# Performance work log

Hardware: AMD Instinct MI355X
Metric: run time of the kernel (lower is better)

The kernel has to match this reference:

```python
import jax, jax.numpy as jnp
import numpy as np
from jax import lax

BN_EPS = 1e-5


def setup_inputs() -> dict:
    key = jax.random.key(0)
    k = jax.random.split(key, 7)
    B, H, W = 128, 224, 224
    return {
        "x": jax.random.normal(k[0], (B, 1, H, W), dtype=jnp.float32),
        "conv_w": jax.random.normal(k[1], (16, 1, 5, 5), dtype=jnp.float32) * 0.1,
        "conv_b": jax.random.normal(k[2], (16,), dtype=jnp.float32) * 0.1,
        "gamma": jax.random.uniform(k[3], (16,), dtype=jnp.float32, minval=0.5, maxval=1.5),
        "beta": jax.random.normal(k[4], (16,), dtype=jnp.float32) * 0.1,
        "run_mean": jax.random.normal(k[5], (16,), dtype=jnp.float32) * 0.1,
        "run_var": jax.random.uniform(k[6], (16,), dtype=jnp.float32, minval=0.5, maxval=1.5),
    }


def reference(x, conv_w, conv_b, gamma, beta, run_mean, run_var):
    # Conv2d(1,16,5,stride=1,padding=2): NCHW x OIHW -> NCHW
    y = lax.conv_general_dilated(
        x, conv_w, window_strides=(1, 1), padding=[(2, 2), (2, 2)],
        dimension_numbers=("NCHW", "OIHW", "NCHW"))
    y = y + conv_b[None, :, None, None]
    # BatchNorm2d(16) in inference form with running stats
    scale = gamma * lax.rsqrt(run_var + BN_EPS)
    y = y * scale[None, :, None, None] + (beta - run_mean * scale)[None, :, None, None]
    # ReLU
    y = jnp.maximum(y, 0.0)
    # MaxPool2d(kernel=2, stride=2)
    out = lax.reduce_window(y, -jnp.inf, lax.max,
                            window_dimensions=(1, 1, 2, 2),
                            window_strides=(1, 1, 2, 2),
                            padding="VALID")
    return out  # [B, 16, H/2, W/2]
```

## Files before the change

kernel.cpp:

```cpp
#include <hip/hip_runtime.h>
#include <stdint.h>

#define TILE_P 16
#define TILE_C 32
#define HALO 2
#define IN_TILE 36
#define IMG 224
#define OUT_DIM 112
#define NCH 16

typedef __fp16 half2_t __attribute__((ext_vector_type(2)));

#define WS_WPAIRS 32

__global__ void prep_kernel(const float* __restrict__ conv_w,
                            const float* __restrict__ conv_b,
                            const float* __restrict__ gamma,
                            const float* __restrict__ beta,
                            const float* __restrict__ run_mean,
                            const float* __restrict__ run_var,
                            uint32_t* __restrict__ ws)
{
    int ch = threadIdx.x;
    if (ch >= NCH) return;
    float s = gamma[ch] * rsqrtf(run_var[ch] + 1e-5f);
    float t = fmaf(s, conv_b[ch] - run_mean[ch], beta[ch]);
    float2* st = (float2*)ws;
    st[ch] = make_float2(s, t);

    uint32_t* wp = ws + WS_WPAIRS + ch * 20;
    const float* w = conv_w + ch * 25;
    for (int r = 0; r < 5; ++r) {
        half2_t A = __builtin_amdgcn_cvt_pkrtz(w[r*5+0], w[r*5+1]);
        half2_t B = __builtin_amdgcn_cvt_pkrtz(w[r*5+2], w[r*5+3]);
        half2_t C = __builtin_amdgcn_cvt_pkrtz(w[r*5+4], 0.f);
        half2_t D = __builtin_amdgcn_cvt_pkrtz(0.f, w[r*5+4]);
        wp[r*4+0] = __builtin_bit_cast(uint32_t, A);
        wp[r*4+1] = __builtin_bit_cast(uint32_t, B);
        wp[r*4+2] = __builtin_bit_cast(uint32_t, C);
        wp[r*4+3] = __builtin_bit_cast(uint32_t, D);
    }
}

__global__ __launch_bounds__(256, 4)
void conv_bn_relu_pool(const float* __restrict__ x,
                       const uint32_t* __restrict__ ws,
                       float* __restrict__ out)
{
    __shared__ float smem[IN_TILE * IN_TILE];
    const int tid = threadIdx.x;
    const int b  = blockIdx.z;
    const int ty = blockIdx.y * TILE_C;
    const int tx = blockIdx.x * TILE_C;

    const float* xb = x + (size_t)b * IMG * IMG;

    for (int i = tid; i < IN_TILE * IN_TILE; i += 256) {
        int r = i / IN_TILE, c = i - r * IN_TILE;
        int gy = ty - HALO + r, gx = tx - HALO + c;
        float v = 0.f;
        if ((unsigned)gy < IMG && (unsigned)gx < IMG) v = xb[gy * IMG + gx];
        smem[i] = v;
    }
    __syncthreads();

    const int px = tid & 15;
    const int py = tid >> 4;

    const int base = (py * 2) * IN_TILE + px * 2;
    half2_t h2[6][5];
    #pragma unroll
    for (int r = 0; r < 6; ++r) {
        float p0 = smem[base + r * IN_TILE + 0];
        float p1 = smem[base + r * IN_TILE + 1];
        float p2 = smem[base + r * IN_TILE + 2];
        float p3 = smem[base + r * IN_TILE + 3];
        float p4 = smem[base + r * IN_TILE + 4];
        float p5 = smem[base + r * IN_TILE + 5];
        h2[r][0] = __builtin_amdgcn_cvt_pkrtz(p0, p1);
        h2[r][1] = __builtin_amdgcn_cvt_pkrtz(p1, p2);
        h2[r][2] = __builtin_amdgcn_cvt_pkrtz(p2, p3);
        h2[r][3] = __builtin_amdgcn_cvt_pkrtz(p3, p4);
        h2[r][4] = __builtin_amdgcn_cvt_pkrtz(p4, p5);
    }

    const int oy = blockIdx.y * TILE_P + py;
    const int ox = blockIdx.x * TILE_P + px;
    float* outb = out + (size_t)b * NCH * (OUT_DIM * OUT_DIM) + oy * OUT_DIM + ox;

    const float2* st = (const float2*)ws;

    #pragma unroll
    for (int ch = 0; ch < NCH; ++ch) {
        const uint32_t* wp = ws + WS_WPAIRS + ch * 20;
        float a00 = 0.f, a01 = 0.f, a10 = 0.f, a11 = 0.f;
        #pragma unroll
        for (int r = 0; r < 5; ++r) {
            half2_t A = __builtin_bit_cast(half2_t, wp[r*4+0]);
            half2_t B = __builtin_bit_cast(half2_t, wp[r*4+1]);
            half2_t C = __builtin_bit_cast(half2_t, wp[r*4+2]);
            half2_t D = __builtin_bit_cast(half2_t, wp[r*4+3]);
            a00 = __builtin_amdgcn_fdot2(h2[r][0], A, a00, false);
            a00 = __builtin_amdgcn_fdot2(h2[r][2], B, a00, false);
            a00 = __builtin_amdgcn_fdot2(h2[r][4], C, a00, false);
            a01 = __builtin_amdgcn_fdot2(h2[r][1], A, a01, false);
            a01 = __builtin_amdgcn_fdot2(h2[r][3], B, a01, false);
            a01 = __builtin_amdgcn_fdot2(h2[r][4], D, a01, false);
            a10 = __builtin_amdgcn_fdot2(h2[r+1][0], A, a10, false);
            a10 = __builtin_amdgcn_fdot2(h2[r+1][2], B, a10, false);
            a10 = __builtin_amdgcn_fdot2(h2[r+1][4], C, a10, false);
            a11 = __builtin_amdgcn_fdot2(h2[r+1][1], A, a11, false);
            a11 = __builtin_amdgcn_fdot2(h2[r+1][3], B, a11, false);
            a11 = __builtin_amdgcn_fdot2(h2[r+1][4], D, a11, false);
        }
        float m = fmaxf(fmaxf(a00, a01), fmaxf(a10, a11));
        float2 s_t = st[ch];
        float y = fmaxf(fmaf(m, s_t.x, s_t.y), 0.f);
        outb[ch * (OUT_DIM * OUT_DIM)] = y;
    }
}

extern "C" void kernel_launch(void* const* d_in, const int* in_sizes, int n_in,
                              void* d_out, int out_size, void* d_ws, size_t ws_size,
                              hipStream_t stream) {
    const float* x        = (const float*)d_in[0];
    const float* conv_w   = (const float*)d_in[1];
    const float* conv_b   = (const float*)d_in[2];
    const float* gamma    = (const float*)d_in[3];
    const float* beta     = (const float*)d_in[4];
    const float* run_mean = (const float*)d_in[5];
    const float* run_var  = (const float*)d_in[6];
    float* out = (float*)d_out;
    uint32_t* ws = (uint32_t*)d_ws;

    prep_kernel<<<1, 64, 0, stream>>>(conv_w, conv_b, gamma, beta, run_mean, run_var, ws);

    dim3 grid(IMG / TILE_C, IMG / TILE_C, 128);
    dim3 block(256);
    conv_bn_relu_pool<<<grid, block, 0, stream>>>(x, ws, out);
}
```

Measured before the change: 175.0 us.

## Precompute packed fp16 pixel pairs in LDS and process channels in groups

The block now converts the input tile once into a shared table of packed fp16 adjacent-pixel pairs, instead of each thread converting its own overlapping 6x6 window. The channel loop is restructured into four non-unrolled groups of four channels; within each group the thread reloads its pairs from LDS per filter row. The launch-bounds occupancy hint is also dropped. The aim is to cut redundant conversions and register pressure, at the cost of an extra barrier, more LDS space and repeated LDS reads across groups.

```diff
diff --git a/kernel.cpp b/kernel.cpp
--- a/kernel.cpp
+++ b/kernel.cpp
@@ -8,6 +8,7 @@
 #define IMG 224
 #define OUT_DIM 112
 #define NCH 16
+#define PAIR_STRIDE 40
 
 typedef __fp16 half2_t __attribute__((ext_vector_type(2)));
 
@@ -42,12 +43,18 @@
     }
 }
 
-__global__ __launch_bounds__(256, 4)
+__device__ __forceinline__ half2_t ld_pair(const uint32_t* p) {
+    return __builtin_bit_cast(half2_t, *p);
+}
+
+__global__ __launch_bounds__(256)
 void conv_bn_relu_pool(const float* __restrict__ x,
                        const uint32_t* __restrict__ ws,
                        float* __restrict__ out)
 {
-    __shared__ float smem[IN_TILE * IN_TILE];
+    __shared__ float T[IN_TILE * IN_TILE];
+    __shared__ uint32_t P[IN_TILE * PAIR_STRIDE];
+
     const int tid = threadIdx.x;
     const int b  = blockIdx.z;
     const int ty = blockIdx.y * TILE_C;
@@ -60,29 +67,20 @@
         int gy = ty - HALO + r, gx = tx - HALO + c;
         float v = 0.f;
         if ((unsigned)gy < IMG && (unsigned)gx < IMG) v = xb[gy * IMG + gx];
-        smem[i] = v;
+        T[i] = v;
+    }
+    __syncthreads();
+
+    for (int i = tid; i < IN_TILE * (IN_TILE - 1); i += 256) {
+        int r = i / (IN_TILE - 1), c = i - r * (IN_TILE - 1);
+        half2_t h = __builtin_amdgcn_cvt_pkrtz(T[r * IN_TILE + c], T[r * IN_TILE + c + 1]);
+        P[r * PAIR_STRIDE + c] = __builtin_bit_cast(uint32_t, h);
     }
     __syncthreads();
 
     const int px = tid & 15;
     const int py = tid >> 4;
-
-    const int base = (py * 2) * IN_TILE + px * 2;
-    half2_t h2[6][5];
-    #pragma unroll
-    for (int r = 0; r < 6; ++r) {
-        float p0 = smem[base + r * IN_TILE + 0];
-        float p1 = smem[base + r * IN_TILE + 1];
-        float p2 = smem[base + r * IN_TILE + 2];
-        float p3 = smem[base + r * IN_TILE + 3];
-        float p4 = smem[base + r * IN_TILE + 4];
-        float p5 = smem[base + r * IN_TILE + 5];
-        h2[r][0] = __builtin_amdgcn_cvt_pkrtz(p0, p1);
-        h2[r][1] = __builtin_amdgcn_cvt_pkrtz(p1, p2);
-        h2[r][2] = __builtin_amdgcn_cvt_pkrtz(p2, p3);
-        h2[r][3] = __builtin_amdgcn_cvt_pkrtz(p3, p4);
-        h2[r][4] = __builtin_amdgcn_cvt_pkrtz(p4, p5);
-    }
+    const uint32_t* prow = P + (2 * py) * PAIR_STRIDE + 2 * px;
 
     const int oy = blockIdx.y * TILE_P + py;
     const int ox = blockIdx.x * TILE_P + px;
@@ -90,33 +88,54 @@
 
     const float2* st = (const float2*)ws;
 
-    #pragma unroll
-    for (int ch = 0; ch < NCH; ++ch) {
-        const uint32_t* wp = ws + WS_WPAIRS + ch * 20;
-        float a00 = 0.f, a01 = 0.f, a10 = 0.f, a11 = 0.f;
+    #pragma unroll 1
+    for (int g = 0; g < 4; ++g) {
+        const uint32_t* wp = ws + WS_WPAIRS + g * 80;
+        float acc[4][4];
+        #pragma unroll
+        for (int i = 0; i < 4; ++i)
+            #pragma unroll
+            for (int j = 0; j < 4; ++j) acc[i][j] = 0.f;
+
         #pragma unroll
         for (int r = 0; r < 5; ++r) {
-            half2_t A = __builtin_bit_cast(half2_t, wp[r*4+0]);
-            half2_t B = __builtin_bit_cast(half2_t, wp[r*4+1]);
-            half2_t C = __builtin_bit_cast(half2_t, wp[r*4+2]);
-            half2_t D = __builtin_bit_cast(half2_t, wp[r*4+3]);
-            a00 = __builtin_amdgcn_fdot2(h2[r][0], A, a00, false);
-            a00 = __builtin_amdgcn_fdot2(h2[r][2], B, a00, false);
-            a00 = __builtin_amdgcn_fdot2(h2[r][4], C, a00, false);
-            a01 = __builtin_amdgcn_fdot2(h2[r][1], A, a01, false);
-            a01 = __builtin_amdgcn_fdot2(h2[r][3], B, a01, false);
-            a01 = __builtin_amdgcn_fdot2(h2[r][4], D, a01, false);
-            a10 = __builtin_amdgcn_fdot2(h2[r+1][0], A, a10, false);
-            a10 = __builtin_amdgcn_fdot2(h2[r+1][2], B, a10, false);
-            a10 = __builtin_amdgcn_fdot2(h2[r+1][4], C, a10, false);
-            a11 = __builtin_amdgcn_fdot2(h2[r+1][1], A, a11, false);
-            a11 = __builtin_amdgcn_fdot2(h2[r+1][3], B, a11, false);
-            a11 = __builtin_amdgcn_fdot2(h2[r+1][4], D, a11, false);
+            const uint32_t* p0 = prow + r * PAIR_STRIDE;
+            const uint32_t* p1 = p0 + PAIR_STRIDE;
+            half2_t q00 = ld_pair(p0 + 0), q01 = ld_pair(p0 + 1);
+            half2_t q02 = ld_pair(p0 + 2), q03 = ld_pair(p0 + 3);
+            half2_t q04 = ld_pair(p0 + 4);
+            half2_t q10 = ld_pair(p1 + 0), q11 = ld_pair(p1 + 1);
+            half2_t q12 = ld_pair(p1 + 2), q13 = ld_pair(p1 + 3);
+            half2_t q14 = ld_pair(p1 + 4);
+            #pragma unroll
+            for (int i = 0; i < 4; ++i) {
+                half2_t A = __builtin_bit_cast(half2_t, wp[i*20 + r*4 + 0]);
+                half2_t B = __builtin_bit_cast(half2_t, wp[i*20 + r*4 + 1]);
+                half2_t C = __builtin_bit_cast(half2_t, wp[i*20 + r*4 + 2]);
+                half2_t D = __builtin_bit_cast(half2_t, wp[i*20 + r*4 + 3]);
+                acc[i][0] = __builtin_amdgcn_fdot2(q00, A,
+                            __builtin_amdgcn_fdot2(q02, B,
+                            __builtin_amdgcn_fdot2(q04, C, acc[i][0], false), false), false);
+                acc[i][1] = __builtin_amdgcn_fdot2(q01, A,
+                            __builtin_amdgcn_fdot2(q03, B,
+                            __builtin_amdgcn_fdot2(q04, D, acc[i][1], false), false), false);
+                acc[i][2] = __builtin_amdgcn_fdot2(q10, A,
+                            __builtin_amdgcn_fdot2(q12, B,
+                            __builtin_amdgcn_fdot2(q14, C, acc[i][2], false), false), false);
+                acc[i][3] = __builtin_amdgcn_fdot2(q11, A,
+                            __builtin_amdgcn_fdot2(q13, B,
+                            __builtin_amdgcn_fdot2(q14, D, acc[i][3], false), false), false);
+            }
         }
-        float m = fmaxf(fmaxf(a00, a01), fmaxf(a10, a11));
-        float2 s_t = st[ch];
-        float y = fmaxf(fmaf(m, s_t.x, s_t.y), 0.f);
-        outb[ch * (OUT_DIM * OUT_DIM)] = y;
+
+        #pragma unroll
+        for (int i = 0; i < 4; ++i) {
+            int ch = g * 4 + i;
+            float m = fmaxf(fmaxf(acc[i][0], acc[i][1]), fmaxf(acc[i][2], acc[i][3]));
+            float2 s_t = st[ch];
+            float y = fmaxf(fmaf(m, s_t.x, s_t.y), 0.f);
+            outb[ch * (OUT_DIM * OUT_DIM)] = y;
+        }
     }
 }
 
```

Result: no change. 173.4 us (-0.9%).
